# Performance work log

Hardware: AMD Instinct MI355X
Metric: run time of the kernel (lower is better)

The kernel has to match this reference:

```python
import jax, jax.numpy as jnp
import numpy as np

N, D, K = 65536, 512, 5


def setup_inputs() -> dict:
    key = jax.random.key(0)
    k0, k1, k2, k3, k4 = jax.random.split(key, 5)
    x = jax.random.normal(k0, (N, D), dtype=jnp.float32)
    is_protected = jax.random.randint(k1, (N,), 0, 2) > 0  # bool mask
    alpha_p = jax.random.uniform(k2, (D,), dtype=jnp.float32, minval=0.9, maxval=1.1)
    classif_w = jax.random.normal(k3, (K, 1), dtype=jnp.float32)
    centroids = jax.random.normal(k4, (K, D), dtype=jnp.float32)
    return {"x": x, "is_protected": is_protected, "alpha_p": alpha_p,
            "classif_w": classif_w, "centroids": centroids}


def reference(x, is_protected, alpha_p, classif_w, centroids):
    # NOTE: original torch forward applies alpha_p to both the protected and
    # non-protected rows (alpha_np is unused), so the mask split is a no-op
    # and we compute the mapping over all rows at once.
    # distances: sum_d alpha_d * (x_nd - c_kd)^2  -> (n, k)
    diff2 = (x[:, None, :] - centroids[None, :, :]) ** 2  # (n, k, d)
    dist = jnp.einsum("nkd,d->nk", diff2, alpha_p)
    mapping = jax.nn.softmax(dist, axis=-1)              # (n, k)
    reconstructed = mapping @ centroids                  # (n, d)
    pred = (mapping @ jax.nn.sigmoid(classif_w)).ravel() # (n,)
    return mapping, reconstructed, pred
```

## Files before the change

kernel.cpp:

```cpp
#include <hip/hip_runtime.h>
#include <math.h>

#define LFR_N 65536
#define LFR_D 512
#define LFR_K 5
#define ROWS  4

__global__ __launch_bounds__(256) void lfr_kernel(
    const float* __restrict__ x,
    const float* __restrict__ alpha,
    const float* __restrict__ w,
    const float* __restrict__ cent,
    float* __restrict__ out_map,
    float* __restrict__ out_rec,
    float* __restrict__ out_pred)
{
    const int lane           = threadIdx.x & 63;
    const int wave_in_block  = threadIdx.x >> 6;
    const int waves_per_blk  = blockDim.x >> 6;
    const int wave_id        = blockIdx.x * waves_per_blk + wave_in_block;
    const int num_waves      = gridDim.x * waves_per_blk;

    const int d0 = lane * 8;

    float al[8];
    {
        float4 a0 = *(const float4*)(alpha + d0);
        float4 a1 = *(const float4*)(alpha + d0 + 4);
        al[0]=a0.x; al[1]=a0.y; al[2]=a0.z; al[3]=a0.w;
        al[4]=a1.x; al[5]=a1.y; al[6]=a1.z; al[7]=a1.w;
    }
    float c[LFR_K][8];
    #pragma unroll
    for (int k = 0; k < LFR_K; ++k) {
        float4 c0 = *(const float4*)(cent + k * LFR_D + d0);
        float4 c1 = *(const float4*)(cent + k * LFR_D + d0 + 4);
        c[k][0]=c0.x; c[k][1]=c0.y; c[k][2]=c0.z; c[k][3]=c0.w;
        c[k][4]=c1.x; c[k][5]=c1.y; c[k][6]=c1.z; c[k][7]=c1.w;
    }
    float sigw[LFR_K];
    #pragma unroll
    for (int k = 0; k < LFR_K; ++k)
        sigw[k] = 1.0f / (1.0f + __expf(-w[k]));

    for (int rb = wave_id * ROWS; rb < LFR_N; rb += num_waves * ROWS) {
        float xv[ROWS][8];
        #pragma unroll
        for (int r = 0; r < ROWS; ++r) {
            const float* xr = x + (size_t)(rb + r) * LFR_D + d0;
            float4 x0 = *(const float4*)(xr);
            float4 x1 = *(const float4*)(xr + 4);
            xv[r][0]=x0.x; xv[r][1]=x0.y; xv[r][2]=x0.z; xv[r][3]=x0.w;
            xv[r][4]=x1.x; xv[r][5]=x1.y; xv[r][6]=x1.z; xv[r][7]=x1.w;
        }

        float dist[ROWS][LFR_K];
        #pragma unroll
        for (int r = 0; r < ROWS; ++r) {
            #pragma unroll
            for (int k = 0; k < LFR_K; ++k) {
                float acc = 0.0f;
                #pragma unroll
                for (int j = 0; j < 8; ++j) {
                    float df = xv[r][j] - c[k][j];
                    acc = fmaf(al[j] * df, df, acc);
                }
                dist[r][k] = acc;
            }
        }

        #pragma unroll
        for (int off = 32; off > 0; off >>= 1) {
            #pragma unroll
            for (int r = 0; r < ROWS; ++r)
                #pragma unroll
                for (int k = 0; k < LFR_K; ++k)
                    dist[r][k] += __shfl_xor(dist[r][k], off);
        }

        float m[ROWS][LFR_K];
        #pragma unroll
        for (int r = 0; r < ROWS; ++r) {
            float mx = dist[r][0];
            #pragma unroll
            for (int k = 1; k < LFR_K; ++k) mx = fmaxf(mx, dist[r][k]);
            float s = 0.0f;
            #pragma unroll
            for (int k = 0; k < LFR_K; ++k) { m[r][k] = __expf(dist[r][k] - mx); s += m[r][k]; }
            float inv = 1.0f / s;
            #pragma unroll
            for (int k = 0; k < LFR_K; ++k) m[r][k] *= inv;
        }

        #pragma unroll
        for (int r = 0; r < ROWS; ++r) {
            float rv[8];
            #pragma unroll
            for (int j = 0; j < 8; ++j) {
                float acc = m[r][0] * c[0][j];
                #pragma unroll
                for (int k = 1; k < LFR_K; ++k) acc = fmaf(m[r][k], c[k][j], acc);
                rv[j] = acc;
            }
            float* rr = out_rec + (size_t)(rb + r) * LFR_D + d0;
            *(float4*)(rr)     = make_float4(rv[0], rv[1], rv[2], rv[3]);
            *(float4*)(rr + 4) = make_float4(rv[4], rv[5], rv[6], rv[7]);
        }

        if (lane < ROWS * LFR_K) {
            int r = lane / LFR_K, k = lane - r * LFR_K;
            out_map[(size_t)(rb + r) * LFR_K + k] = m[r][k];
        }
        if (lane >= 32 && lane < 32 + ROWS) {
            int r = lane - 32;
            float p = 0.0f;
            #pragma unroll
            for (int k = 0; k < LFR_K; ++k) p = fmaf(m[r][k], sigw[k], p);
            out_pred[rb + r] = p;
        }
    }
}

extern "C" void kernel_launch(void* const* d_in, const int* in_sizes, int n_in,
                              void* d_out, int out_size, void* d_ws, size_t ws_size,
                              hipStream_t stream) {
    const float* x     = (const float*)d_in[0];
    const float* alpha = (const float*)d_in[2];
    const float* w     = (const float*)d_in[3];
    const float* cent  = (const float*)d_in[4];

    float* out   = (float*)d_out;
    float* o_map = out;
    float* o_rec = out + (size_t)LFR_N * LFR_K;
    float* o_prd = out + (size_t)LFR_N * LFR_K + (size_t)LFR_N * LFR_D;

    dim3 grid(2048), block(256);
    lfr_kernel<<<grid, block, 0, stream>>>(x, alpha, w, cent, o_map, o_rec, o_prd);
}
```

Baseline: 266.1 us.

## Drop grid-stride loop, one row-group per wave with x loads issued first

Replaces the persistent grid-stride loop with a launch that gives each wave exactly one 4-row group (4096 blocks). The x row loads now come before the alpha and centroid loads, so the bandwidth-bound x fetch overlaps with the constant setup. The map and pred outputs are written by one lane per row, using a float4 plus a scalar store. The aim is to raise memory-level parallelism and hide load latency. The cost is repeating the per-wave constant loads and sigmoid setup for twice as many waves, and the float4 map store is not 16-byte aligned.

```diff
diff --git a/kernel.cpp b/kernel.cpp
--- a/kernel.cpp
+++ b/kernel.cpp
@@ -15,13 +15,21 @@
     float* __restrict__ out_rec,
     float* __restrict__ out_pred)
 {
-    const int lane           = threadIdx.x & 63;
-    const int wave_in_block  = threadIdx.x >> 6;
-    const int waves_per_blk  = blockDim.x >> 6;
-    const int wave_id        = blockIdx.x * waves_per_blk + wave_in_block;
-    const int num_waves      = gridDim.x * waves_per_blk;
+    const int lane          = threadIdx.x & 63;
+    const int wave_in_block = threadIdx.x >> 6;
+    const int wave_id       = blockIdx.x * (blockDim.x >> 6) + wave_in_block;
+    const int rb            = wave_id * ROWS;
+    if (rb >= LFR_N) return;
 
     const int d0 = lane * 8;
+
+    float4 xl[ROWS][2];
+    #pragma unroll
+    for (int r = 0; r < ROWS; ++r) {
+        const float* xr = x + (size_t)(rb + r) * LFR_D + d0;
+        xl[r][0] = *(const float4*)(xr);
+        xl[r][1] = *(const float4*)(xr + 4);
+    }
 
     float al[8];
     {
@@ -43,79 +51,74 @@
     for (int k = 0; k < LFR_K; ++k)
         sigw[k] = 1.0f / (1.0f + __expf(-w[k]));
 
-    for (int rb = wave_id * ROWS; rb < LFR_N; rb += num_waves * ROWS) {
-        float xv[ROWS][8];
+    float xv[ROWS][8];
+    #pragma unroll
+    for (int r = 0; r < ROWS; ++r) {
+        xv[r][0]=xl[r][0].x; xv[r][1]=xl[r][0].y; xv[r][2]=xl[r][0].z; xv[r][3]=xl[r][0].w;
+        xv[r][4]=xl[r][1].x; xv[r][5]=xl[r][1].y; xv[r][6]=xl[r][1].z; xv[r][7]=xl[r][1].w;
+    }
+    float dist[ROWS][LFR_K];
+    #pragma unroll
+    for (int r = 0; r < ROWS; ++r) {
         #pragma unroll
-        for (int r = 0; r < ROWS; ++r) {
-            const float* xr = x + (size_t)(rb + r) * LFR_D + d0;
-            float4 x0 = *(const float4*)(xr);
-            float4 x1 = *(const float4*)(xr + 4);
-            xv[r][0]=x0.x; xv[r][1]=x0.y; xv[r][2]=x0.z; xv[r][3]=x0.w;
-            xv[r][4]=x1.x; xv[r][5]=x1.y; xv[r][6]=x1.z; xv[r][7]=x1.w;
-        }
-
-        float dist[ROWS][LFR_K];
-        #pragma unroll
-        for (int r = 0; r < ROWS; ++r) {
-            #pragma unroll
-            for (int k = 0; k < LFR_K; ++k) {
-                float acc = 0.0f;
-                #pragma unroll
-                for (int j = 0; j < 8; ++j) {
-                    float df = xv[r][j] - c[k][j];
-                    acc = fmaf(al[j] * df, df, acc);
-                }
-                dist[r][k] = acc;
-            }
-        }
-
-        #pragma unroll
-        for (int off = 32; off > 0; off >>= 1) {
-            #pragma unroll
-            for (int r = 0; r < ROWS; ++r)
-                #pragma unroll
-                for (int k = 0; k < LFR_K; ++k)
-                    dist[r][k] += __shfl_xor(dist[r][k], off);
-        }
-
-        float m[ROWS][LFR_K];
-        #pragma unroll
-        for (int r = 0; r < ROWS; ++r) {
-            float mx = dist[r][0];
-            #pragma unroll
-            for (int k = 1; k < LFR_K; ++k) mx = fmaxf(mx, dist[r][k]);
-            float s = 0.0f;
-            #pragma unroll
-            for (int k = 0; k < LFR_K; ++k) { m[r][k] = __expf(dist[r][k] - mx); s += m[r][k]; }
-            float inv = 1.0f / s;
-            #pragma unroll
-            for (int k = 0; k < LFR_K; ++k) m[r][k] *= inv;
-        }
-
-        #pragma unroll
-        for (int r = 0; r < ROWS; ++r) {
-            float rv[8];
+        for (int k = 0; k < LFR_K; ++k) {
+            float acc = 0.0f;
             #pragma unroll
             for (int j = 0; j < 8; ++j) {
-                float acc = m[r][0] * c[0][j];
-                #pragma unroll
-                for (int k = 1; k < LFR_K; ++k) acc = fmaf(m[r][k], c[k][j], acc);
-                rv[j] = acc;
+                float df = xv[r][j] - c[k][j];
+                acc = fmaf(al[j] * df, df, acc);
             }
-            float* rr = out_rec + (size_t)(rb + r) * LFR_D + d0;
-            *(float4*)(rr)     = make_float4(rv[0], rv[1], rv[2], rv[3]);
-            *(float4*)(rr + 4) = make_float4(rv[4], rv[5], rv[6], rv[7]);
+            dist[r][k] = acc;
         }
+    }
 
-        if (lane < ROWS * LFR_K) {
-            int r = lane / LFR_K, k = lane - r * LFR_K;
-            out_map[(size_t)(rb + r) * LFR_K + k] = m[r][k];
+    #pragma unroll
+    for (int off = 32; off > 0; off >>= 1) {
+        #pragma unroll
+        for (int r = 0; r < ROWS; ++r)
+            #pragma unroll
+            for (int k = 0; k < LFR_K; ++k)
+                dist[r][k] += __shfl_xor(dist[r][k], off);
+    }
+
+    float m[ROWS][LFR_K];
+    #pragma unroll
+    for (int r = 0; r < ROWS; ++r) {
+        float mx = dist[r][0];
+        #pragma unroll
+        for (int k = 1; k < LFR_K; ++k) mx = fmaxf(mx, dist[r][k]);
+        float s = 0.0f;
+        #pragma unroll
+        for (int k = 0; k < LFR_K; ++k) { m[r][k] = __expf(dist[r][k] - mx); s += m[r][k]; }
+        float inv = 1.0f / s;
+        #pragma unroll
+        for (int k = 0; k < LFR_K; ++k) m[r][k] *= inv;
+    }
+
+    #pragma unroll
+    for (int r = 0; r < ROWS; ++r) {
+        float rv[8];
+        #pragma unroll
+        for (int j = 0; j < 8; ++j) {
+            float acc = m[r][0] * c[0][j];
+            #pragma unroll
+            for (int k = 1; k < LFR_K; ++k) acc = fmaf(m[r][k], c[k][j], acc);
+            rv[j] = acc;
         }
-        if (lane >= 32 && lane < 32 + ROWS) {
-            int r = lane - 32;
-            float p = 0.0f;
+        float* rr = out_rec + (size_t)(rb + r) * LFR_D + d0;
+        *(float4*)(rr)     = make_float4(rv[0], rv[1], rv[2], rv[3]);
+        *(float4*)(rr + 4) = make_float4(rv[4], rv[5], rv[6], rv[7]);
+    }
+
+    #pragma unroll
+    for (int r = 0; r < ROWS; ++r) {
+        if (lane == r) {
+            float* mp = out_map + (size_t)(rb + r) * LFR_K;
+            *(float4*)(mp) = make_float4(m[r][0], m[r][1], m[r][2], m[r][3]);
+            mp[4] = m[r][4];
+            float p = m[r][0] * sigw[0];
             #pragma unroll
-            for (int k = 0; k < LFR_K; ++k) p = fmaf(m[r][k], sigw[k], p);
+            for (int k = 1; k < LFR_K; ++k) p = fmaf(m[r][k], sigw[k], p);
             out_pred[rb + r] = p;
         }
     }
@@ -134,6 +137,6 @@
     float* o_rec = out + (size_t)LFR_N * LFR_K;
     float* o_prd = out + (size_t)LFR_N * LFR_K + (size_t)LFR_N * LFR_D;
 
-    dim3 grid(2048), block(256);
+    dim3 grid(LFR_N / (4 * ROWS)), block(256);
     lfr_kernel<<<grid, block, 0, stream>>>(x, alpha, w, cent, o_map, o_rec, o_prd);
 }
```

Measured after the change: 241.9 us. -9.1%, faster.

## Expand distance algebraically and stage x tiles through double-buffered LDS

Applied to the files above, without the earlier changes.

The weighted squared distance is rewritten as sum(alpha*c^2) - 2*x·(alpha*c). The per-row x^2 term is dropped because softmax is invariant to a per-row constant. Each thread now accumulates dot products for one row half over double-buffered 32-column LDS chunks, which removes the per-row cross-lane shuffle reductions of the old wave-per-row design. Mapping values go through shared memory so a separate wave-wide pass can write the reconstruction coalesced. In exchange it uses a fixed 512-block grid with many __syncthreads and large LDS use, which may limit occupancy and latency hiding.

```diff
diff --git a/kernel.cpp b/kernel.cpp
--- a/kernel.cpp
+++ b/kernel.cpp
@@ -4,9 +4,14 @@
 #define LFR_N 65536
 #define LFR_D 512
 #define LFR_K 5
-#define ROWS  4
+#define TPB   256
+#define RPB   128
+#define NBLK  (LFR_N / RPB)
+#define CH    32
+#define NCH   (LFR_D / CH)
+#define STRIDE (CH + 4)
 
-__global__ __launch_bounds__(256) void lfr_kernel(
+__global__ __launch_bounds__(TPB) void lfr_kernel(
     const float* __restrict__ x,
     const float* __restrict__ alpha,
     const float* __restrict__ w,
@@ -15,109 +20,159 @@
     float* __restrict__ out_rec,
     float* __restrict__ out_pred)
 {
-    const int lane           = threadIdx.x & 63;
-    const int wave_in_block  = threadIdx.x >> 6;
-    const int waves_per_blk  = blockDim.x >> 6;
-    const int wave_id        = blockIdx.x * waves_per_blk + wave_in_block;
-    const int num_waves      = gridDim.x * waves_per_blk;
+    __shared__ float xbuf[2][RPB * STRIDE];
+    __shared__ float cbuf[LFR_K * LFR_D];
 
-    const int d0 = lane * 8;
+    const int t   = threadIdx.x;
+    const int wv  = t >> 6;
+    const int l   = t & 63;
+    const int rb0 = blockIdx.x * RPB;
 
-    float al[8];
+    const float4* __restrict__ x4 = (const float4*)x;
+
     {
-        float4 a0 = *(const float4*)(alpha + d0);
-        float4 a1 = *(const float4*)(alpha + d0 + 4);
-        al[0]=a0.x; al[1]=a0.y; al[2]=a0.z; al[3]=a0.w;
-        al[4]=a1.x; al[5]=a1.y; al[6]=a1.z; al[7]=a1.w;
+        const float4* c4 = (const float4*)cent;
+        const float4* a4 = (const float4*)alpha;
+        #pragma unroll
+        for (int i = 0; i < 3; ++i) {
+            int f = i * TPB + t;
+            if (f < LFR_K * LFR_D / 4) {
+                int k = f >> 7, d4 = f & 127;
+                float4 cv = c4[k * 128 + d4];
+                float4 av = a4[d4];
+                float4 o;
+                o.x = cv.x * av.x; o.y = cv.y * av.y;
+                o.z = cv.z * av.z; o.w = cv.w * av.w;
+                ((float4*)cbuf)[f] = o;
+            }
+        }
     }
-    float c[LFR_K][8];
+
+    #pragma unroll
+    for (int i = 0; i < 4; ++i) {
+        int f = i * TPB + t;
+        int r = f >> 3, q = f & 7;
+        float4 v = x4[(size_t)(rb0 + r) * 128 + q];
+        ((float4*)&xbuf[0][r * STRIDE])[q] = v;
+    }
+    __syncthreads();
+
+    float Bk[LFR_K];
+    {
+        const int db = l * 8;
+        #pragma unroll
+        for (int k = 0; k < LFR_K; ++k) {
+            float s = 0.0f;
+            #pragma unroll
+            for (int j = 0; j < 8; ++j)
+                s = fmaf(cbuf[k * LFR_D + db + j], cent[k * LFR_D + db + j], s);
+            Bk[k] = s;
+        }
+        #pragma unroll
+        for (int off = 32; off > 0; off >>= 1)
+            #pragma unroll
+            for (int k = 0; k < LFR_K; ++k)
+                Bk[k] += __shfl_xor(Bk[k], off);
+    }
+
+    const int R = wv * 32 + (l & 31);
+    const int h = l >> 5;
+    float dot[LFR_K] = {0.f, 0.f, 0.f, 0.f, 0.f};
+
+    for (int c = 0; c < NCH; ++c) {
+        const int cur = c & 1;
+        float4 pf[4];
+        if (c + 1 < NCH) {
+            #pragma unroll
+            for (int i = 0; i < 4; ++i) {
+                int f = i * TPB + t, r = f >> 3, q = f & 7;
+                pf[i] = x4[(size_t)(rb0 + r) * 128 + (c + 1) * 8 + q];
+            }
+        }
+        const float* xb = &xbuf[cur][R * STRIDE + 16 * h];
+        #pragma unroll
+        for (int j = 0; j < 4; ++j) {
+            float4 xq = ((const float4*)xb)[j];
+            #pragma unroll
+            for (int k = 0; k < LFR_K; ++k) {
+                float4 cq = ((const float4*)&cbuf[k * LFR_D + c * CH + 16 * h])[j];
+                dot[k] = fmaf(xq.x, cq.x, dot[k]);
+                dot[k] = fmaf(xq.y, cq.y, dot[k]);
+                dot[k] = fmaf(xq.z, cq.z, dot[k]);
+                dot[k] = fmaf(xq.w, cq.w, dot[k]);
+            }
+        }
+        if (c + 1 < NCH) {
+            #pragma unroll
+            for (int i = 0; i < 4; ++i) {
+                int f = i * TPB + t, r = f >> 3, q = f & 7;
+                ((float4*)&xbuf[cur ^ 1][r * STRIDE])[q] = pf[i];
+            }
+        }
+        __syncthreads();
+    }
+
+    #pragma unroll
+    for (int k = 0; k < LFR_K; ++k)
+        dot[k] += __shfl_xor(dot[k], 32);
+
+    float dist[LFR_K], m[LFR_K];
+    #pragma unroll
+    for (int k = 0; k < LFR_K; ++k) dist[k] = Bk[k] - 2.0f * dot[k];
+    float mx = dist[0];
+    #pragma unroll
+    for (int k = 1; k < LFR_K; ++k) mx = fmaxf(mx, dist[k]);
+    float s = 0.0f;
+    #pragma unroll
+    for (int k = 0; k < LFR_K; ++k) { m[k] = __expf(dist[k] - mx); s += m[k]; }
+    float inv = 1.0f / s;
+    #pragma unroll
+    for (int k = 0; k < LFR_K; ++k) m[k] *= inv;
+
+    float* mb = &xbuf[0][0];
+    if (h == 0) {
+        float* mp = out_map + (size_t)(rb0 + R) * LFR_K;
+        mp[0] = m[0]; mp[1] = m[1]; mp[2] = m[2]; mp[3] = m[3]; mp[4] = m[4];
+        float p = 0.0f;
+        #pragma unroll
+        for (int k = 0; k < LFR_K; ++k) {
+            float sw = 1.0f / (1.0f + __expf(-w[k]));
+            p = fmaf(m[k], sw, p);
+        }
+        out_pred[rb0 + R] = p;
+        #pragma unroll
+        for (int k = 0; k < LFR_K; ++k) mb[R * 8 + k] = m[k];
+    }
+    __syncthreads();
+
+    float cc[LFR_K][8];
+    const int d0 = l * 8;
     #pragma unroll
     for (int k = 0; k < LFR_K; ++k) {
-        float4 c0 = *(const float4*)(cent + k * LFR_D + d0);
-        float4 c1 = *(const float4*)(cent + k * LFR_D + d0 + 4);
-        c[k][0]=c0.x; c[k][1]=c0.y; c[k][2]=c0.z; c[k][3]=c0.w;
-        c[k][4]=c1.x; c[k][5]=c1.y; c[k][6]=c1.z; c[k][7]=c1.w;
+        float4 a = *(const float4*)(cent + k * LFR_D + d0);
+        float4 b = *(const float4*)(cent + k * LFR_D + d0 + 4);
+        cc[k][0]=a.x; cc[k][1]=a.y; cc[k][2]=a.z; cc[k][3]=a.w;
+        cc[k][4]=b.x; cc[k][5]=b.y; cc[k][6]=b.z; cc[k][7]=b.w;
     }
-    float sigw[LFR_K];
-    #pragma unroll
-    for (int k = 0; k < LFR_K; ++k)
-        sigw[k] = 1.0f / (1.0f + __expf(-w[k]));
-
-    for (int rb = wave_id * ROWS; rb < LFR_N; rb += num_waves * ROWS) {
-        float xv[ROWS][8];
+    const int r0 = wv * 32;
+    #pragma unroll 2
+    for (int rr = 0; rr < 32; ++rr) {
+        const int r = r0 + rr;
+        float m0 = mb[r * 8 + 0], m1 = mb[r * 8 + 1], m2 = mb[r * 8 + 2],
+              m3 = mb[r * 8 + 3], m4 = mb[r * 8 + 4];
+        float rv[8];
         #pragma unroll
-        for (int r = 0; r < ROWS; ++r) {
-            const float* xr = x + (size_t)(rb + r) * LFR_D + d0;
-            float4 x0 = *(const float4*)(xr);
-            float4 x1 = *(const float4*)(xr + 4);
-            xv[r][0]=x0.x; xv[r][1]=x0.y; xv[r][2]=x0.z; xv[r][3]=x0.w;
-            xv[r][4]=x1.x; xv[r][5]=x1.y; xv[r][6]=x1.z; xv[r][7]=x1.w;
+        for (int j = 0; j < 8; ++j) {
+            float acc = m0 * cc[0][j];
+            acc = fmaf(m1, cc[1][j], acc);
+            acc = fmaf(m2, cc[2][j], acc);
+            acc = fmaf(m3, cc[3][j], acc);
+            acc = fmaf(m4, cc[4][j], acc);
+            rv[j] = acc;
         }
-
-        float dist[ROWS][LFR_K];
-        #pragma unroll
-        for (int r = 0; r < ROWS; ++r) {
-            #pragma unroll
-            for (int k = 0; k < LFR_K; ++k) {
-                float acc = 0.0f;
-                #pragma unroll
-                for (int j = 0; j < 8; ++j) {
-                    float df = xv[r][j] - c[k][j];
-                    acc = fmaf(al[j] * df, df, acc);
-                }
-                dist[r][k] = acc;
-            }
-        }
-
-        #pragma unroll
-        for (int off = 32; off > 0; off >>= 1) {
-            #pragma unroll
-            for (int r = 0; r < ROWS; ++r)
-                #pragma unroll
-                for (int k = 0; k < LFR_K; ++k)
-                    dist[r][k] += __shfl_xor(dist[r][k], off);
-        }
-
-        float m[ROWS][LFR_K];
-        #pragma unroll
-        for (int r = 0; r < ROWS; ++r) {
-            float mx = dist[r][0];
-            #pragma unroll
-            for (int k = 1; k < LFR_K; ++k) mx = fmaxf(mx, dist[r][k]);
-            float s = 0.0f;
-            #pragma unroll
-            for (int k = 0; k < LFR_K; ++k) { m[r][k] = __expf(dist[r][k] - mx); s += m[r][k]; }
-            float inv = 1.0f / s;
-            #pragma unroll
-            for (int k = 0; k < LFR_K; ++k) m[r][k] *= inv;
-        }
-
-        #pragma unroll
-        for (int r = 0; r < ROWS; ++r) {
-            float rv[8];
-            #pragma unroll
-            for (int j = 0; j < 8; ++j) {
-                float acc = m[r][0] * c[0][j];
-                #pragma unroll
-                for (int k = 1; k < LFR_K; ++k) acc = fmaf(m[r][k], c[k][j], acc);
-                rv[j] = acc;
-            }
-            float* rr = out_rec + (size_t)(rb + r) * LFR_D + d0;
-            *(float4*)(rr)     = make_float4(rv[0], rv[1], rv[2], rv[3]);
-            *(float4*)(rr + 4) = make_float4(rv[4], rv[5], rv[6], rv[7]);
-        }
-
-        if (lane < ROWS * LFR_K) {
-            int r = lane / LFR_K, k = lane - r * LFR_K;
-            out_map[(size_t)(rb + r) * LFR_K + k] = m[r][k];
-        }
-        if (lane >= 32 && lane < 32 + ROWS) {
-            int r = lane - 32;
-            float p = 0.0f;
-            #pragma unroll
-            for (int k = 0; k < LFR_K; ++k) p = fmaf(m[r][k], sigw[k], p);
-            out_pred[rb + r] = p;
-        }
+        float* orow = out_rec + (size_t)(rb0 + r) * LFR_D + d0;
+        ((float4*)orow)[0] = make_float4(rv[0], rv[1], rv[2], rv[3]);
+        ((float4*)orow)[1] = make_float4(rv[4], rv[5], rv[6], rv[7]);
     }
 }
 
@@ -134,6 +189,6 @@
     float* o_rec = out + (size_t)LFR_N * LFR_K;
     float* o_prd = out + (size_t)LFR_N * LFR_K + (size_t)LFR_N * LFR_D;
 
-    dim3 grid(2048), block(256);
+    dim3 grid(NBLK), block(TPB);
     lfr_kernel<<<grid, block, 0, stream>>>(x, alpha, w, cent, o_map, o_rec, o_prd);
 }
```

Measured after the change: 310.1 us. 16.5% more time.
